# Performance work log

Hardware: AMD Instinct MI355X
Metric: run time of the kernel (lower is better)

The kernel has to match this reference:

```python
import jax, jax.numpy as jnp
import numpy as np

N_DOMAINS = 4          # number of unique domain labels in d
NUM_PROJ = 50          # hard-coded in DiscriminativeSlicedWasserstein.__init__
P_POW = 2              # hard-coded p=2


def setup_inputs() -> dict:
    key = jax.random.key(0)
    k1, k2, k3 = jax.random.split(key, 3)
    N, IN_DIM, OUT_DIM = 32768, 2048, 512
    z = jax.random.normal(k1, (N, IN_DIM), dtype=jnp.float32)
    W = jax.random.normal(k2, (IN_DIM, OUT_DIM), dtype=jnp.float32) * 0.02
    b = jnp.zeros((OUT_DIM,), dtype=jnp.float32)
    # random projections on the unit sphere (rows normalized), as in rand_projections
    P = jax.random.normal(k3, (NUM_PROJ, OUT_DIM), dtype=jnp.float32)
    P = P / jnp.sqrt(jnp.sum(P * P, axis=1, keepdims=True))
    # sorted, equal-count domain labels -> grouping becomes a static reshape
    d = jnp.repeat(jnp.arange(N_DOMAINS, dtype=jnp.int32), N // N_DOMAINS)
    return {"z": z, "W": W, "b": b, "P": P, "d": d}


def reference(z, W, b, P, d):
    # z = self.D(z): linear discriminator
    h = z @ W + b                                   # [N, out_dim]
    per = h.shape[0] // N_DOMAINS
    groups = h.reshape(N_DOMAINS, per, -1)          # [G, n, out_dim] (d is sorted equal-count)
    # project each group onto the random directions: z.matmul(P.T)
    proj = jnp.einsum('gnd,kd->gnk', groups, P)     # [G, n, num_proj]
    # sort along the sample axis (torch sorts each projection's values)
    srt = jnp.sort(proj, axis=1)                    # [G, n, num_proj]
    # all domain pairs (itertools.combinations); equal group sizes => mean of
    # per-pair means == mean over the stacked pair differences
    ii, jj = np.triu_indices(N_DOMAINS, k=1)
    diff = srt[jj] - srt[ii]                        # [n_pairs, n, num_proj]
    loss = jnp.mean(diff ** P_POW)
    return loss
```

## Files before the change

kernel.cpp:

```cpp
#include <hip/hip_runtime.h>

#define NROWS 32768
#define KDIM  2048
#define DDIM  512
#define NPROJ 50
#define NDOM  4
#define NPER  8192
#define BNPAD 64

typedef __attribute__((ext_vector_type(8))) short short8v;
typedef __attribute__((ext_vector_type(4))) float f32x4;

__device__ inline ushort bf16_rne(float x) {
  union { float f; unsigned u; } v; v.f = x;
  unsigned r = v.u + 0x7FFF + ((v.u >> 16) & 1);
  return (ushort)(r >> 16);
}
__device__ inline float bf16_f32(ushort h) {
  union { unsigned u; float f; } v; v.u = ((unsigned)h) << 16;
  return v.f;
}

__global__ __launch_bounds__(256) void wp_kernel(const float* __restrict__ W,
                                                 const float* __restrict__ b,
                                                 const float* __restrict__ P,
                                                 ushort* __restrict__ Bpk,
                                                 float* __restrict__ bp) {
  int idx = blockIdx.x * 256 + threadIdx.x;
  if (idx >= (KDIM + 1) * BNPAD) return;
  int i = idx >> 6;
  int c = idx & 63;
  float acc = 0.f;
  if (c < NPROJ) {
    const float4* row = (const float4*)((i < KDIM) ? (W + (size_t)i * DDIM) : b);
    const float4* pr  = (const float4*)(P + (size_t)c * DDIM);
#pragma unroll 4
    for (int d = 0; d < DDIM / 4; ++d) {
      float4 w = row[d], p = pr[d];
      acc += w.x * p.x + w.y * p.y + w.z * p.z + w.w * p.w;
    }
  }
  if (i < KDIM) {
    int tg = i >> 5, kb = (i >> 3) & 3, e = i & 7;
    int m = c & 15, cf = c >> 4;
    size_t pos = (size_t)(tg * 4 + cf) * 1024 + (kb * 16 + m) * 8 + e;
    ushort h = bf16_rne(acc);
    Bpk[pos]       = h;
    Bpk[pos + 512] = bf16_rne(acc - bf16_f32(h));
  } else {
    bp[c] = acc;
  }
}

__device__ __forceinline__ void split8_trunc(const float4 f0, const float4 f1,
                                             short8v& hi, short8v& lo) {
  const float a[8] = {f0.x, f0.y, f0.z, f0.w, f1.x, f1.y, f1.z, f1.w};
  union { unsigned u[4]; short8v s; } H, L;
#pragma unroll
  for (int p = 0; p < 4; ++p) {
    float a0 = a[2 * p], a1 = a[2 * p + 1];
    unsigned u0 = __float_as_uint(a0), u1 = __float_as_uint(a1);
    H.u[p] = __builtin_amdgcn_perm(u1, u0, 0x07060302);
    float l0 = a0 - __uint_as_float(u0 & 0xFFFF0000u);
    float l1 = a1 - __uint_as_float(u1 & 0xFFFF0000u);
    L.u[p] = __builtin_amdgcn_perm(__float_as_uint(l1), __float_as_uint(l0), 0x07060302);
  }
  hi = H.s; lo = L.s;
}

__device__ __forceinline__ void gload16(const float* g, float* l) {
  __builtin_amdgcn_global_load_lds(
      (const __attribute__((address_space(1))) unsigned int*)(unsigned long long)g,
      (__attribute__((address_space(3))) unsigned int*)(unsigned int)(unsigned long long)l,
      16, 0, 0);
}

__global__ __launch_bounds__(256) void gemm_mfma(const float* __restrict__ z,
                                                 const ushort* __restrict__ Bpk,
                                                 const float* __restrict__ bp,
                                                 float* __restrict__ projT) {
  __shared__ __align__(16) float A_lds[2][4096];
  __shared__ __align__(16) float B_lds[2][4096];

  const int tid  = threadIdx.x;
  const int lane = tid & 63;
  const int wave = tid >> 6;
  const int m    = lane & 15;
  const int kb   = lane >> 4;
  const int row0 = blockIdx.x * 64;

  const float* gsrcA[4];
  const float* gsrcB[4];
  const float* Bf = (const float*)Bpk;
#pragma unroll
  for (int ii = 0; ii < 4; ++ii) {
    const int i    = wave * 4 + ii;
    const int trow = i * 4 + (lane >> 4);
    const int q    = (lane & 15) ^ (trow & 15);
    gsrcA[ii] = z + (size_t)(row0 + trow) * KDIM + q * 4;
    gsrcB[ii] = Bf + (size_t)i * 256 + lane * 4;
  }

#define STAGE(buf_, t_)                                                  \
  {                                                                      \
    _Pragma("unroll")                                                    \
    for (int ii = 0; ii < 4; ++ii) {                                     \
      const int i = wave * 4 + ii;                                       \
      gload16(gsrcA[ii] + (t_) * 64, &A_lds[buf_][i * 256]);             \
      gload16(gsrcB[ii] + (size_t)(t_) * 4096, &B_lds[buf_][i * 256]);   \
    }                                                                    \
  }

  f32x4 acc[4] = {(f32x4)0.f, (f32x4)0.f, (f32x4)0.f, (f32x4)0.f};

  STAGE(0, 0);
  __syncthreads();

#pragma unroll 2
  for (int t = 0; t < 32; ++t) {
    const int buf = t & 1;

    const float* base = &A_lds[buf][(wave * 16 + m) * 64];
    float4 f[2][2];
#pragma unroll
    for (int ks = 0; ks < 2; ++ks) {
      const int q0 = ks * 8 + kb * 2;
      f[ks][0] = *(const float4*)(base + ((q0 ^ m) * 4));
      f[ks][1] = *(const float4*)(base + (((q0 + 1) ^ m) * 4));
    }
    short8v bh[2][4], bl[2][4];
    const ushort* Bu = (const ushort*)&B_lds[buf][0];
#pragma unroll
    for (int ks = 0; ks < 2; ++ks)
#pragma unroll
      for (int cf = 0; cf < 4; ++cf) {
        const ushort* fb = Bu + (ks * 4 + cf) * 1024 + lane * 8;
        bh[ks][cf] = *(const short8v*)fb;
        bl[ks][cf] = *(const short8v*)(fb + 512);
      }
    __builtin_amdgcn_sched_barrier(0);

    if (t < 31) STAGE(buf ^ 1, t + 1);
    __builtin_amdgcn_sched_barrier(0);

    short8v ah[2], al[2];
#pragma unroll
    for (int ks = 0; ks < 2; ++ks)
      split8_trunc(f[ks][0], f[ks][1], ah[ks], al[ks]);

#pragma unroll
    for (int ks = 0; ks < 2; ++ks)
#pragma unroll
      for (int cf = 0; cf < 4; ++cf) {
        acc[cf] = __builtin_amdgcn_mfma_f32_16x16x32_bf16(ah[ks], bh[ks][cf], acc[cf], 0, 0, 0);
        acc[cf] = __builtin_amdgcn_mfma_f32_16x16x32_bf16(al[ks], bh[ks][cf], acc[cf], 0, 0, 0);
        acc[cf] = __builtin_amdgcn_mfma_f32_16x16x32_bf16(ah[ks], bl[ks][cf], acc[cf], 0, 0, 0);
      }

    __syncthreads();
  }
#undef STAGE

  const int g     = row0 >> 13;
  const int nbase = (row0 & (NPER - 1)) + wave * 16;
#pragma unroll
  for (int cf = 0; cf < 4; ++cf) {
    const int col = cf * 16 + m;
    if (col < NPROJ) {
      const float bj = bp[col];
      float* dst = projT + (size_t)(g * NPROJ + col) * NPER + nbase + kb * 4;
      dst[0] = acc[cf][0] + bj;
      dst[1] = acc[cf][1] + bj;
      dst[2] = acc[cf][2] + bj;
      dst[3] = acc[cf][3] + bj;
    }
  }
}

#define CE(a, b, asc) { float x_ = v[a], y_ = v[b]; \
  if ((asc) ? (x_ > y_) : (x_ < y_)) { v[a] = y_; v[b] = x_; } }

__device__ inline int swz(int i) { return i ^ (((i >> 5) & 7) << 2); }
#define SPAD 8192

template <int JMAX>
__device__ inline void wave_merge(float v[8], int t, int k) {
  const bool asc = (((t << 3) & k) == 0);
#pragma unroll
  for (int j = JMAX; j >= 8; j >>= 1) {
    const int d = j >> 3;
    const bool keepmin = (asc != ((t & d) != 0));
#pragma unroll
    for (int e = 0; e < 8; ++e) {
      float o = __shfl_xor(v[e], d, 64);
      v[e] = keepmin ? fminf(v[e], o) : fmaxf(v[e], o);
    }
  }
  CE(0, 4, asc); CE(1, 5, asc); CE(2, 6, asc); CE(3, 7, asc);
  CE(0, 2, asc); CE(1, 3, asc); CE(4, 6, asc); CE(5, 7, asc);
  CE(0, 1, asc); CE(2, 3, asc); CE(4, 5, asc); CE(6, 7, asc);
}

__global__ __launch_bounds__(1024) void sort_cols(float* __restrict__ projT) {
  __shared__ __align__(16) float sA[SPAD];
  __shared__ __align__(16) float sB[SPAD];
  float* col = projT + (size_t)blockIdx.x * NPER;
  const int t  = threadIdx.x;
  const int i0 = t << 3;
  float v[8];

  *(float4*)&v[0] = *(const float4*)(col + i0);
  *(float4*)&v[4] = *(const float4*)(col + i0 + 4);

  CE(0, 1, true);  CE(2, 3, false); CE(4, 5, true);  CE(6, 7, false);
  CE(0, 2, true);  CE(1, 3, true);  CE(4, 6, false); CE(5, 7, false);
  CE(0, 1, true);  CE(2, 3, true);  CE(4, 5, false); CE(6, 7, false);
  {
    bool d8 = (t & 1) == 0;
    CE(0, 4, d8); CE(1, 5, d8); CE(2, 6, d8); CE(3, 7, d8);
    CE(0, 2, d8); CE(1, 3, d8); CE(4, 6, d8); CE(5, 7, d8);
    CE(0, 1, d8); CE(2, 3, d8); CE(4, 5, d8); CE(6, 7, d8);
  }

  wave_merge<8>(v, t, 16);
  wave_merge<16>(v, t, 32);
  wave_merge<32>(v, t, 64);
  wave_merge<64>(v, t, 128);
  wave_merge<128>(v, t, 256);
  wave_merge<256>(v, t, 512);

  *(float4*)&sA[swz(i0)]     = *(float4*)&v[0];
  *(float4*)&sA[swz(i0 + 4)] = *(float4*)&v[4];
  __syncthreads();
  int cur = 0;

  for (int k = 1024; k <= NPER; k <<= 1) {
    const bool asc = ((i0 & k) == 0);
    for (int j = k >> 1; j >= 512; j >>= 1) {
      const float* src = cur ? sB : sA;
      float*       dst = cur ? sA : sB;
      const int ip = i0 ^ j;
      float4 a0 = *(const float4*)&src[swz(i0)];
      float4 a1 = *(const float4*)&src[swz(i0 + 4)];
      float4 b0 = *(const float4*)&src[swz(ip)];
      float4 b1 = *(const float4*)&src[swz(ip + 4)];
      const bool keepmin = (asc != ((i0 & j) != 0));
      float4 r0, r1;
      if (keepmin) {
        r0.x = fminf(a0.x, b0.x); r0.y = fminf(a0.y, b0.y); r0.z = fminf(a0.z, b0.z); r0.w = fminf(a0.w, b0.w);
        r1.x = fminf(a1.x, b1.x); r1.y = fminf(a1.y, b1.y); r1.z = fminf(a1.z, b1.z); r1.w = fminf(a1.w, b1.w);
      } else {
        r0.x = fmaxf(a0.x, b0.x); r0.y = fmaxf(a0.y, b0.y); r0.z = fmaxf(a0.z, b0.z); r0.w = fmaxf(a0.w, b0.w);
        r1.x = fmaxf(a1.x, b1.x); r1.y = fmaxf(a1.y, b1.y); r1.z = fmaxf(a1.z, b1.z); r1.w = fmaxf(a1.w, b1.w);
      }
      *(float4*)&dst[swz(i0)]     = r0;
      *(float4*)&dst[swz(i0 + 4)] = r1;
      __syncthreads();
      cur ^= 1;
      *(float4*)&v[0] = r0;
      *(float4*)&v[4] = r1;
    }
    wave_merge<256>(v, t, k);
    if (k != NPER) {
      float* d2 = cur ? sB : sA;
      *(float4*)&d2[swz(i0)]     = *(float4*)&v[0];
      *(float4*)&d2[swz(i0 + 4)] = *(float4*)&v[4];
      __syncthreads();
    }
  }

  *(float4*)(col + i0)     = *(float4*)&v[0];
  *(float4*)(col + i0 + 4) = *(float4*)&v[4];
}

__global__ __launch_bounds__(256) void reduce_k(const float* __restrict__ projT,
                                                float* __restrict__ partial) {
  const int k  = blockIdx.x;
  const int nc = blockIdx.y;
  const int n  = nc * 1024 + threadIdx.x * 4;
  const float4 x0 = *(const float4*)(projT + (size_t)(0 * NPROJ + k) * NPER + n);
  const float4 x1 = *(const float4*)(projT + (size_t)(1 * NPROJ + k) * NPER + n);
  const float4 x2 = *(const float4*)(projT + (size_t)(2 * NPROJ + k) * NPER + n);
  const float4 x3 = *(const float4*)(projT + (size_t)(3 * NPROJ + k) * NPER + n);
  const float a0[4] = {x0.x, x0.y, x0.z, x0.w};
  const float a1[4] = {x1.x, x1.y, x1.z, x1.w};
  const float a2[4] = {x2.x, x2.y, x2.z, x2.w};
  const float a3[4] = {x3.x, x3.y, x3.z, x3.w};
  float local = 0.f;
#pragma unroll
  for (int e = 0; e < 4; ++e) {
    float d01 = a0[e] - a1[e], d02 = a0[e] - a2[e], d03 = a0[e] - a3[e];
    float d12 = a1[e] - a2[e], d13 = a1[e] - a3[e], d23 = a2[e] - a3[e];
    local += d01 * d01 + d02 * d02 + d03 * d03 + d12 * d12 + d13 * d13 + d23 * d23;
  }
#pragma unroll
  for (int o = 32; o > 0; o >>= 1) local += __shfl_down(local, o, 64);
  __shared__ float red[4];
  if ((threadIdx.x & 63) == 0) red[threadIdx.x >> 6] = local;
  __syncthreads();
  if (threadIdx.x == 0) partial[nc * NPROJ + k] = red[0] + red[1] + red[2] + red[3];
}

__global__ __launch_bounds__(512) void final_k(const float* __restrict__ partial,
                                               float* __restrict__ out) {
  const int t = threadIdx.x;
  float v = (t < 8 * NPROJ) ? partial[t] : 0.f;
#pragma unroll
  for (int o = 32; o > 0; o >>= 1) v += __shfl_down(v, o, 64);
  __shared__ float red[8];
  if ((t & 63) == 0) red[t >> 6] = v;
  __syncthreads();
  if (t == 0) {
    float s = 0.f;
#pragma unroll
    for (int w = 0; w < 8; ++w) s += red[w];
    out[0] = s * (1.0f / (6.0f * NPER * NPROJ));
  }
}

extern "C" void kernel_launch(void* const* d_in, const int* in_sizes, int n_in,
                              void* d_out, int out_size, void* d_ws, size_t ws_size,
                              hipStream_t stream) {
  const float* z = (const float*)d_in[0];
  const float* W = (const float*)d_in[1];
  const float* b = (const float*)d_in[2];
  const float* P = (const float*)d_in[3];

  float*  projT   = (float*)d_ws;
  ushort* Bpk     = (ushort*)(projT + (size_t)NDOM * NPROJ * NPER);
  float*  bp      = (float*)(Bpk + (size_t)2 * BNPAD * KDIM);
  float*  partial = bp + BNPAD;

  wp_kernel<<<((KDIM + 1) * BNPAD + 255) / 256, 256, 0, stream>>>(W, b, P, Bpk, bp);
  gemm_mfma<<<NROWS / 64, 256, 0, stream>>>(z, Bpk, bp, projT);
  sort_cols<<<NDOM * NPROJ, 1024, 0, stream>>>(projT);
  reduce_k<<<dim3(NPROJ, 8), 256, 0, stream>>>(projT, partial);
  final_k<<<1, 512, 0, stream>>>(partial, (float*)d_out);
}
```

Measured before the change: 127.1 us.

## Split GEMM K dimension across two blocks and sum partials in sort

The projection GEMM now runs as a split-K launch with two K halves per row tile, doubling the grid to 1024 blocks. Each half writes its own partial buffer, and the sort kernel adds the two partials when it loads each column. The K step also shrinks from 64 to 32, so per-block LDS drops and more blocks can be resident at once. The cost is an extra partial buffer in workspace memory plus its write and read traffic, and more loop iterations per element of work. If the workspace is too small, the code falls back to the single-slice path.

```diff
diff --git a/kernel.cpp b/kernel.cpp
--- a/kernel.cpp
+++ b/kernel.cpp
@@ -75,12 +75,15 @@
       16, 0, 0);
 }
 
+template <int KS>
 __global__ __launch_bounds__(256) void gemm_mfma(const float* __restrict__ z,
                                                  const ushort* __restrict__ Bpk,
                                                  const float* __restrict__ bp,
-                                                 float* __restrict__ projT) {
-  __shared__ __align__(16) float A_lds[2][4096];
-  __shared__ __align__(16) float B_lds[2][4096];
+                                                 float* __restrict__ part) {
+  constexpr int KSLICE = KDIM / KS;
+  constexpr int NSTEP  = KSLICE / 32;
+  __shared__ __align__(16) float A_lds[2][64 * 32];
+  __shared__ __align__(16) float B_lds[2][2048];
 
   const int tid  = threadIdx.x;
   const int lane = tid & 63;
@@ -88,27 +91,29 @@
   const int m    = lane & 15;
   const int kb   = lane >> 4;
   const int row0 = blockIdx.x * 64;
-
-  const float* gsrcA[4];
-  const float* gsrcB[4];
+  const int ksb  = (KS == 2) ? blockIdx.y : 0;
+  const int k0   = ksb * KSLICE;
+
+  const float* gsrcA[2];
+  const float* gsrcB[2];
   const float* Bf = (const float*)Bpk;
 #pragma unroll
-  for (int ii = 0; ii < 4; ++ii) {
-    const int i    = wave * 4 + ii;
-    const int trow = i * 4 + (lane >> 4);
-    const int q    = (lane & 15) ^ (trow & 15);
-    gsrcA[ii] = z + (size_t)(row0 + trow) * KDIM + q * 4;
-    gsrcB[ii] = Bf + (size_t)i * 256 + lane * 4;
-  }
-
-#define STAGE(buf_, t_)                                                  \
-  {                                                                      \
-    _Pragma("unroll")                                                    \
-    for (int ii = 0; ii < 4; ++ii) {                                     \
-      const int i = wave * 4 + ii;                                       \
-      gload16(gsrcA[ii] + (t_) * 64, &A_lds[buf_][i * 256]);             \
-      gload16(gsrcB[ii] + (size_t)(t_) * 4096, &B_lds[buf_][i * 256]);   \
-    }                                                                    \
+  for (int ii = 0; ii < 2; ++ii) {
+    const int j = wave * 2 + ii;
+    const int r = j * 8 + (lane >> 3);
+    const int q = (lane & 7) ^ (r & 7);
+    gsrcA[ii] = z + (size_t)(row0 + r) * KDIM + k0 + q * 4;
+    gsrcB[ii] = Bf + (size_t)(k0 >> 5) * 2048 + j * 256 + lane * 4;
+  }
+
+#define STAGE(buf_, t_)                                                 \
+  {                                                                     \
+    _Pragma("unroll")                                                   \
+    for (int ii = 0; ii < 2; ++ii) {                                    \
+      const int j = wave * 2 + ii;                                      \
+      gload16(gsrcA[ii] + (t_) * 32, &A_lds[buf_][j * 256]);            \
+      gload16(gsrcB[ii] + (size_t)(t_) * 2048, &B_lds[buf_][j * 256]);  \
+    }                                                                   \
   }
 
   f32x4 acc[4] = {(f32x4)0.f, (f32x4)0.f, (f32x4)0.f, (f32x4)0.f};
@@ -117,58 +122,48 @@
   __syncthreads();
 
 #pragma unroll 2
-  for (int t = 0; t < 32; ++t) {
+  for (int t = 0; t < NSTEP; ++t) {
     const int buf = t & 1;
 
-    const float* base = &A_lds[buf][(wave * 16 + m) * 64];
-    float4 f[2][2];
-#pragma unroll
-    for (int ks = 0; ks < 2; ++ks) {
-      const int q0 = ks * 8 + kb * 2;
-      f[ks][0] = *(const float4*)(base + ((q0 ^ m) * 4));
-      f[ks][1] = *(const float4*)(base + (((q0 + 1) ^ m) * 4));
-    }
-    short8v bh[2][4], bl[2][4];
+    const int wr = wave * 16 + m;
+    const float* base = &A_lds[buf][wr * 32];
+    float4 f0 = *(const float4*)(base + (((kb * 2) ^ (wr & 7)) * 4));
+    float4 f1 = *(const float4*)(base + (((kb * 2 + 1) ^ (wr & 7)) * 4));
+    short8v bh[4], bl[4];
     const ushort* Bu = (const ushort*)&B_lds[buf][0];
 #pragma unroll
-    for (int ks = 0; ks < 2; ++ks)
-#pragma unroll
-      for (int cf = 0; cf < 4; ++cf) {
-        const ushort* fb = Bu + (ks * 4 + cf) * 1024 + lane * 8;
-        bh[ks][cf] = *(const short8v*)fb;
-        bl[ks][cf] = *(const short8v*)(fb + 512);
-      }
+    for (int cf = 0; cf < 4; ++cf) {
+      const ushort* fb = Bu + cf * 1024 + lane * 8;
+      bh[cf] = *(const short8v*)fb;
+      bl[cf] = *(const short8v*)(fb + 512);
+    }
     __builtin_amdgcn_sched_barrier(0);
 
-    if (t < 31) STAGE(buf ^ 1, t + 1);
+    if (t < NSTEP - 1) STAGE(buf ^ 1, t + 1);
     __builtin_amdgcn_sched_barrier(0);
 
-    short8v ah[2], al[2];
-#pragma unroll
-    for (int ks = 0; ks < 2; ++ks)
-      split8_trunc(f[ks][0], f[ks][1], ah[ks], al[ks]);
-
-#pragma unroll
-    for (int ks = 0; ks < 2; ++ks)
-#pragma unroll
-      for (int cf = 0; cf < 4; ++cf) {
-        acc[cf] = __builtin_amdgcn_mfma_f32_16x16x32_bf16(ah[ks], bh[ks][cf], acc[cf], 0, 0, 0);
-        acc[cf] = __builtin_amdgcn_mfma_f32_16x16x32_bf16(al[ks], bh[ks][cf], acc[cf], 0, 0, 0);
-        acc[cf] = __builtin_amdgcn_mfma_f32_16x16x32_bf16(ah[ks], bl[ks][cf], acc[cf], 0, 0, 0);
-      }
+    short8v ah, al;
+    split8_trunc(f0, f1, ah, al);
+#pragma unroll
+    for (int cf = 0; cf < 4; ++cf) {
+      acc[cf] = __builtin_amdgcn_mfma_f32_16x16x32_bf16(ah, bh[cf], acc[cf], 0, 0, 0);
+      acc[cf] = __builtin_amdgcn_mfma_f32_16x16x32_bf16(al, bh[cf], acc[cf], 0, 0, 0);
+      acc[cf] = __builtin_amdgcn_mfma_f32_16x16x32_bf16(ah, bl[cf], acc[cf], 0, 0, 0);
+    }
 
     __syncthreads();
   }
 #undef STAGE
 
   const int g     = row0 >> 13;
-  const int nbase = (row0 & (NPER - 1)) + wave * 16;
+  const int nbase = (row0 & (NPER - 1)) + wave * 16 + kb * 4;
 #pragma unroll
   for (int cf = 0; cf < 4; ++cf) {
     const int col = cf * 16 + m;
     if (col < NPROJ) {
-      const float bj = bp[col];
-      float* dst = projT + (size_t)(g * NPROJ + col) * NPER + nbase + kb * 4;
+      const float bj = (ksb == 0) ? bp[col] : 0.f;
+      float* dst = part + (size_t)ksb * (NDOM * NPROJ * NPER) +
+                   (size_t)(g * NPROJ + col) * NPER + nbase;
       dst[0] = acc[cf][0] + bj;
       dst[1] = acc[cf][1] + bj;
       dst[2] = acc[cf][2] + bj;
@@ -201,7 +196,9 @@
   CE(0, 1, asc); CE(2, 3, asc); CE(4, 5, asc); CE(6, 7, asc);
 }
 
-__global__ __launch_bounds__(1024) void sort_cols(float* __restrict__ projT) {
+__global__ __launch_bounds__(1024) void sort_cols(float* __restrict__ projT,
+                                                  const float* __restrict__ part1,
+                                                  int ksum) {
   __shared__ __align__(16) float sA[SPAD];
   __shared__ __align__(16) float sB[SPAD];
   float* col = projT + (size_t)blockIdx.x * NPER;
@@ -211,6 +208,13 @@
 
   *(float4*)&v[0] = *(const float4*)(col + i0);
   *(float4*)&v[4] = *(const float4*)(col + i0 + 4);
+  if (ksum) {
+    const float* c1 = part1 + (size_t)blockIdx.x * NPER;
+    float4 w0 = *(const float4*)(c1 + i0);
+    float4 w1 = *(const float4*)(c1 + i0 + 4);
+    v[0] += w0.x; v[1] += w0.y; v[2] += w0.z; v[3] += w0.w;
+    v[4] += w1.x; v[5] += w1.y; v[6] += w1.z; v[7] += w1.w;
+  }
 
   CE(0, 1, true);  CE(2, 3, false); CE(4, 5, true);  CE(6, 7, false);
   CE(0, 2, true);  CE(1, 3, true);  CE(4, 6, false); CE(5, 7, false);
@@ -326,14 +330,25 @@
   const float* b = (const float*)d_in[2];
   const float* P = (const float*)d_in[3];
 
+  const size_t PELEM = (size_t)NDOM * NPROJ * NPER;
+  const size_t need2 = (2 * PELEM + 2 * (size_t)BNPAD * KDIM / 2
+                        + BNPAD + 8 * NPROJ) * sizeof(float) + 1024;
+  const bool ks2 = (ws_size >= need2);
+
   float*  projT   = (float*)d_ws;
-  ushort* Bpk     = (ushort*)(projT + (size_t)NDOM * NPROJ * NPER);
+  float*  part1   = projT + PELEM;
+  float*  after   = projT + (ks2 ? 2 * PELEM : PELEM);
+  ushort* Bpk     = (ushort*)after;
   float*  bp      = (float*)(Bpk + (size_t)2 * BNPAD * KDIM);
   float*  partial = bp + BNPAD;
 
   wp_kernel<<<((KDIM + 1) * BNPAD + 255) / 256, 256, 0, stream>>>(W, b, P, Bpk, bp);
-  gemm_mfma<<<NROWS / 64, 256, 0, stream>>>(z, Bpk, bp, projT);
-  sort_cols<<<NDOM * NPROJ, 1024, 0, stream>>>(projT);
+  if (ks2) {
+    gemm_mfma<2><<<dim3(NROWS / 64, 2), 256, 0, stream>>>(z, Bpk, bp, projT);
+  } else {
+    gemm_mfma<1><<<dim3(NROWS / 64, 1), 256, 0, stream>>>(z, Bpk, bp, projT);
+  }
+  sort_cols<<<NDOM * NPROJ, 1024, 0, stream>>>(projT, part1, ks2 ? 1 : 0);
   reduce_k<<<dim3(NPROJ, 8), 256, 0, stream>>>(projT, partial);
   final_k<<<1, 512, 0, stream>>>(partial, (float*)d_out);
 }
```

New measurement: 127.0 us. Within noise of the previous version (-0.0%).
